# Optimization experiments

Measured on AMD Instinct MI355X. Metric: run time of the kernel, lower is better.

Reference implementation:

```python
import jax, jax.numpy as jnp
import numpy as np

SINKHORN_ITERS = 4
EPS = 1e-6


def setup_inputs() -> dict:
    key = jax.random.key(0)
    B, T, W, D = 2, 4096, 4, 2048
    k1, k2 = jax.random.split(key, 2)
    x = jax.random.normal(k1, (B, T, W, D), dtype=jnp.float32)
    W_router = jax.random.normal(k2, (W * W + 2 * W, D), dtype=jnp.float32) * 0.02
    b_router = jnp.zeros((W * W + 2 * W,), dtype=jnp.float32)
    return {"x": x, "W_router": W_router, "b_router": b_router}


def _sinkhorn(logits):
    # Bistochastic projection: 4 iterations of alternating row/col normalization.
    def body(w, _):
        w = w / jnp.maximum(w.sum(axis=-1, keepdims=True), EPS)
        w = w / jnp.maximum(w.sum(axis=-2, keepdims=True), EPS)
        return w, None
    w, _ = jax.lax.scan(body, jnp.exp(logits), None, length=SINKHORN_ITERS)
    return w


def reference(x, W_router, b_router):
    B, T, W, D = x.shape
    # router input: mean over the width (stream) dim -> (B, T, D)
    routing_input = x.mean(axis=2)
    raw = routing_input @ W_router.T + b_router          # (B, T, W*W + 2W)
    pre = jax.nn.softmax(raw[..., :W], axis=-1)          # (B, T, W)
    post = jax.nn.softmax(raw[..., W:2 * W], axis=-1)    # (B, T, W)
    res_logits = raw[..., 2 * W:].reshape(B, T, W, W)
    # residual_bias buffer: -2 off-diagonal, +2 on diagonal
    idx = jnp.arange(W)
    bias = jnp.full((W, W), -2.0, dtype=x.dtype).at[idx, idx].set(2.0)
    residual = _sinkhorn(res_logits + bias)              # (B, T, W, W)
    # aggregate streams with pre weights, apply op (identity here)
    aggregated = (x * pre[..., None]).sum(axis=2)        # (B, T, D)
    op_out = aggregated                                  # op = identity
    mixed_residual = jnp.einsum('btij,btjd->btid', residual, x)
    return mixed_residual + post[..., None] * op_out[:, :, None, :]
```

## Files before the change

kernel.cpp:

```cpp
#include <hip/hip_runtime.h>


#define SINKHORN_ITERS 4
#define EPSV 1e-6f

__global__ __launch_bounds__(256, 4) void mchc_fused(
    const float* __restrict__ x,
    const float* __restrict__ Wr,
    const float* __restrict__ br,
    float* __restrict__ out)
{
    const int token = blockIdx.x;
    const int tid   = threadIdx.x;
    const int lane  = tid & 63;
    const int wave  = tid >> 6;

    const float4* __restrict__ x4 = (const float4*)(x + (size_t)token * 8192);
    const float4* __restrict__ w4 = (const float4*)Wr;
    float4*       __restrict__ o4 = (float4*)(out + (size_t)token * 8192);

    float4 xa[4], xb[4];
#pragma unroll
    for (int w = 0; w < 4; ++w) {
        xa[w] = x4[w * 512 + tid];
        xb[w] = x4[w * 512 + 256 + tid];
    }

    float4 sa, sb;
    sa.x = xa[0].x + xa[1].x + xa[2].x + xa[3].x;
    sa.y = xa[0].y + xa[1].y + xa[2].y + xa[3].y;
    sa.z = xa[0].z + xa[1].z + xa[2].z + xa[3].z;
    sa.w = xa[0].w + xa[1].w + xa[2].w + xa[3].w;
    sb.x = xb[0].x + xb[1].x + xb[2].x + xb[3].x;
    sb.y = xb[0].y + xb[1].y + xb[2].y + xb[3].y;
    sb.z = xb[0].z + xb[1].z + xb[2].z + xb[3].z;
    sb.w = xb[0].w + xb[1].w + xb[2].w + xb[3].w;

    float p[24];
#pragma unroll
    for (int k = 0; k < 24; ++k) {
        float4 wa = w4[k * 512 + tid];
        float4 wb = w4[k * 512 + 256 + tid];
        p[k] = sa.x * wa.x + sa.y * wa.y + sa.z * wa.z + sa.w * wa.w
             + sb.x * wb.x + sb.y * wb.y + sb.z * wb.z + sb.w * wb.w;
    }

    __shared__ float red[4][24];
    __shared__ float rawbuf[24];
    __shared__ float Mbuf[16];

#pragma unroll
    for (int k = 0; k < 24; ++k) {
        float v = p[k];
        v += __shfl_xor(v, 1);
        v += __shfl_xor(v, 2);
        v += __shfl_xor(v, 4);
        v += __shfl_xor(v, 8);
        v += __shfl_xor(v, 16);
        v += __shfl_xor(v, 32);
        p[k] = v;
    }
    if (lane == 0) {
#pragma unroll
        for (int k = 0; k < 24; ++k) red[wave][k] = p[k];
    }
    __syncthreads();

    if (tid < 24) {
        float r = red[0][tid] + red[1][tid] + red[2][tid] + red[3][tid];
        rawbuf[tid] = 0.25f * r + br[tid];
    }
    __syncthreads();

    if (tid < 16) {
        const int i = tid >> 2, j = tid & 3;

        float r0 = rawbuf[0], r1 = rawbuf[1], r2 = rawbuf[2], r3 = rawbuf[3];
        float mp = fmaxf(fmaxf(r0, r1), fmaxf(r2, r3));
        float sp = __expf(r0 - mp) + __expf(r1 - mp) + __expf(r2 - mp) + __expf(r3 - mp);
        float pre_j = __expf(rawbuf[j] - mp) / sp;

        float q0 = rawbuf[4], q1 = rawbuf[5], q2 = rawbuf[6], q3 = rawbuf[7];
        float mq = fmaxf(fmaxf(q0, q1), fmaxf(q2, q3));
        float sq = __expf(q0 - mq) + __expf(q1 - mq) + __expf(q2 - mq) + __expf(q3 - mq);
        float post_i = __expf(rawbuf[4 + i] - mq) / sq;

        float w = __expf(rawbuf[8 + tid] + ((i == j) ? 2.0f : -2.0f));
#pragma unroll
        for (int it = 0; it < SINKHORN_ITERS; ++it) {
            float rs = w + __shfl_xor(w, 1);
            rs += __shfl_xor(rs, 2);
            w /= fmaxf(rs, EPSV);
            float cs = w + __shfl_xor(w, 4);
            cs += __shfl_xor(cs, 8);
            w /= fmaxf(cs, EPSV);
        }
        Mbuf[tid] = w + post_i * pre_j;
    }
    __syncthreads();

    float M[16];
#pragma unroll
    for (int m = 0; m < 16; ++m) M[m] = Mbuf[m];

#pragma unroll
    for (int i = 0; i < 4; ++i) {
        float m0 = M[i * 4 + 0], m1 = M[i * 4 + 1], m2 = M[i * 4 + 2], m3 = M[i * 4 + 3];
        float4 oa, ob;
        oa.x = m0 * xa[0].x + m1 * xa[1].x + m2 * xa[2].x + m3 * xa[3].x;
        oa.y = m0 * xa[0].y + m1 * xa[1].y + m2 * xa[2].y + m3 * xa[3].y;
        oa.z = m0 * xa[0].z + m1 * xa[1].z + m2 * xa[2].z + m3 * xa[3].z;
        oa.w = m0 * xa[0].w + m1 * xa[1].w + m2 * xa[2].w + m3 * xa[3].w;
        ob.x = m0 * xb[0].x + m1 * xb[1].x + m2 * xb[2].x + m3 * xb[3].x;
        ob.y = m0 * xb[0].y + m1 * xb[1].y + m2 * xb[2].y + m3 * xb[3].y;
        ob.z = m0 * xb[0].z + m1 * xb[1].z + m2 * xb[2].z + m3 * xb[3].z;
        ob.w = m0 * xb[0].w + m1 * xb[1].w + m2 * xb[2].w + m3 * xb[3].w;
        o4[i * 512 + tid]       = oa;
        o4[i * 512 + 256 + tid] = ob;
    }
}

extern "C" void kernel_launch(void* const* d_in, const int* in_sizes, int n_in,
                              void* d_out, int out_size, void* d_ws, size_t ws_size,
                              hipStream_t stream) {
    const float* x  = (const float*)d_in[0];
    const float* Wr = (const float*)d_in[1];
    const float* br = (const float*)d_in[2];
    float* out = (float*)d_out;

    const int tokens = in_sizes[0] / (4 * 2048);
    mchc_fused<<<dim3(tokens), dim3(256), 0, stream>>>(x, Wr, br, out);
}
```

Measured before the change: 516.4 us.

## Process four tokens per block with register prefetch of next token

Each block now handles four consecutive tokens and prefetches the next token's x into registers while computing the current one. The three block barriers per token become one, using a double-buffered shared reduction array, and every wave computes softmax and Sinkhorn redundantly and broadcasts M by shuffle instead of through shared memory. The aim is to hide global load latency and cut synchronisation and launch overhead. The cost is more registers (two x sets), which may reduce occupancy, and four times fewer blocks; the launch assumes the token count is divisible by four.

```diff
diff --git a/kernel.cpp b/kernel.cpp
--- a/kernel.cpp
+++ b/kernel.cpp
@@ -1,7 +1,7 @@
 #include <hip/hip_runtime.h>
 
 
-#define SINKHORN_ITERS 4
+#define NTOK 4
 #define EPSV 1e-6f
 
 __global__ __launch_bounds__(256, 4) void mchc_fused(
@@ -10,113 +10,126 @@
     const float* __restrict__ br,
     float* __restrict__ out)
 {
-    const int token = blockIdx.x;
-    const int tid   = threadIdx.x;
-    const int lane  = tid & 63;
-    const int wave  = tid >> 6;
+    const int tid  = threadIdx.x;
+    const int lane = tid & 63;
+    const int wave = tid >> 6;
+    const int t0   = blockIdx.x * NTOK;
 
-    const float4* __restrict__ x4 = (const float4*)(x + (size_t)token * 8192);
+    __shared__ float red[2][4][24];
+
     const float4* __restrict__ w4 = (const float4*)Wr;
-    float4*       __restrict__ o4 = (float4*)(out + (size_t)token * 8192);
+
+    float brp[8];
+#pragma unroll
+    for (int k = 0; k < 8; ++k) brp[k] = br[k];
+    const int l16 = lane & 15;
+    const int si = l16 >> 2, sj = l16 & 3;
+    const float brw = br[8 + l16];
 
     float4 xa[4], xb[4];
+    float4 ya[4], yb[4];
+    {
+        const float4* xp = (const float4*)(x + (size_t)t0 * 8192);
 #pragma unroll
-    for (int w = 0; w < 4; ++w) {
-        xa[w] = x4[w * 512 + tid];
-        xb[w] = x4[w * 512 + 256 + tid];
+        for (int w = 0; w < 4; ++w) {
+            xa[w] = xp[w * 512 + tid];
+            xb[w] = xp[w * 512 + 256 + tid];
+        }
     }
 
-    float4 sa, sb;
-    sa.x = xa[0].x + xa[1].x + xa[2].x + xa[3].x;
-    sa.y = xa[0].y + xa[1].y + xa[2].y + xa[3].y;
-    sa.z = xa[0].z + xa[1].z + xa[2].z + xa[3].z;
-    sa.w = xa[0].w + xa[1].w + xa[2].w + xa[3].w;
-    sb.x = xb[0].x + xb[1].x + xb[2].x + xb[3].x;
-    sb.y = xb[0].y + xb[1].y + xb[2].y + xb[3].y;
-    sb.z = xb[0].z + xb[1].z + xb[2].z + xb[3].z;
-    sb.w = xb[0].w + xb[1].w + xb[2].w + xb[3].w;
+#pragma unroll
+    for (int n = 0; n < NTOK; ++n) {
+        const int t = t0 + n;
 
-    float p[24];
+        {
+            const int tn = (n + 1 < NTOK) ? (t + 1) : t;
+            const float4* xp = (const float4*)(x + (size_t)tn * 8192);
 #pragma unroll
-    for (int k = 0; k < 24; ++k) {
-        float4 wa = w4[k * 512 + tid];
-        float4 wb = w4[k * 512 + 256 + tid];
-        p[k] = sa.x * wa.x + sa.y * wa.y + sa.z * wa.z + sa.w * wa.w
-             + sb.x * wb.x + sb.y * wb.y + sb.z * wb.z + sb.w * wb.w;
-    }
+            for (int w = 0; w < 4; ++w) {
+                ya[w] = xp[w * 512 + tid];
+                yb[w] = xp[w * 512 + 256 + tid];
+            }
+        }
 
-    __shared__ float red[4][24];
-    __shared__ float rawbuf[24];
-    __shared__ float Mbuf[16];
+        float4 sa, sb;
+        sa.x = xa[0].x + xa[1].x + xa[2].x + xa[3].x;
+        sa.y = xa[0].y + xa[1].y + xa[2].y + xa[3].y;
+        sa.z = xa[0].z + xa[1].z + xa[2].z + xa[3].z;
+        sa.w = xa[0].w + xa[1].w + xa[2].w + xa[3].w;
+        sb.x = xb[0].x + xb[1].x + xb[2].x + xb[3].x;
+        sb.y = xb[0].y + xb[1].y + xb[2].y + xb[3].y;
+        sb.z = xb[0].z + xb[1].z + xb[2].z + xb[3].z;
+        sb.w = xb[0].w + xb[1].w + xb[2].w + xb[3].w;
 
 #pragma unroll
-    for (int k = 0; k < 24; ++k) {
-        float v = p[k];
-        v += __shfl_xor(v, 1);
-        v += __shfl_xor(v, 2);
-        v += __shfl_xor(v, 4);
-        v += __shfl_xor(v, 8);
-        v += __shfl_xor(v, 16);
-        v += __shfl_xor(v, 32);
-        p[k] = v;
-    }
-    if (lane == 0) {
+        for (int k = 0; k < 24; ++k) {
+            float4 wa = w4[k * 512 + tid];
+            float4 wb = w4[k * 512 + 256 + tid];
+            float v = sa.x * wa.x + sa.y * wa.y + sa.z * wa.z + sa.w * wa.w
+                    + sb.x * wb.x + sb.y * wb.y + sb.z * wb.z + sb.w * wb.w;
+            v += __shfl_xor(v, 1);
+            v += __shfl_xor(v, 2);
+            v += __shfl_xor(v, 4);
+            v += __shfl_xor(v, 8);
+            v += __shfl_xor(v, 16);
+            v += __shfl_xor(v, 32);
+            if (lane == 0) red[n & 1][wave][k] = v;
+        }
+
+        asm volatile("s_waitcnt lgkmcnt(0)\n\ts_barrier" ::: "memory");
+
+        const float* rp = &red[n & 1][0][0];
+        float r[8];
 #pragma unroll
-        for (int k = 0; k < 24; ++k) red[wave][k] = p[k];
-    }
-    __syncthreads();
+        for (int k = 0; k < 8; ++k)
+            r[k] = 0.25f * (rp[k] + rp[24 + k] + rp[48 + k] + rp[72 + k]) + brp[k];
+        float rw = 0.25f * (rp[8 + l16] + rp[32 + l16] + rp[56 + l16] + rp[80 + l16]) + brw;
 
-    if (tid < 24) {
-        float r = red[0][tid] + red[1][tid] + red[2][tid] + red[3][tid];
-        rawbuf[tid] = 0.25f * r + br[tid];
-    }
-    __syncthreads();
+        float mp = fmaxf(fmaxf(r[0], r[1]), fmaxf(r[2], r[3]));
+        float e0 = __expf(r[0] - mp), e1 = __expf(r[1] - mp);
+        float e2 = __expf(r[2] - mp), e3 = __expf(r[3] - mp);
+        float sp = e0 + e1 + e2 + e3;
+        float pre_j = ((sj == 0) ? e0 : (sj == 1) ? e1 : (sj == 2) ? e2 : e3) / sp;
 
-    if (tid < 16) {
-        const int i = tid >> 2, j = tid & 3;
+        float mq = fmaxf(fmaxf(r[4], r[5]), fmaxf(r[6], r[7]));
+        float f0 = __expf(r[4] - mq), f1 = __expf(r[5] - mq);
+        float f2 = __expf(r[6] - mq), f3 = __expf(r[7] - mq);
+        float sq = f0 + f1 + f2 + f3;
+        float post_i = ((si == 0) ? f0 : (si == 1) ? f1 : (si == 2) ? f2 : f3) / sq;
 
-        float r0 = rawbuf[0], r1 = rawbuf[1], r2 = rawbuf[2], r3 = rawbuf[3];
-        float mp = fmaxf(fmaxf(r0, r1), fmaxf(r2, r3));
-        float sp = __expf(r0 - mp) + __expf(r1 - mp) + __expf(r2 - mp) + __expf(r3 - mp);
-        float pre_j = __expf(rawbuf[j] - mp) / sp;
+        float wv = __expf(rw + ((si == sj) ? 2.0f : -2.0f));
+#pragma unroll
+        for (int it = 0; it < 4; ++it) {
+            float rs = wv + __shfl_xor(wv, 1); rs += __shfl_xor(rs, 2);
+            wv /= fmaxf(rs, EPSV);
+            float cs = wv + __shfl_xor(wv, 4); cs += __shfl_xor(cs, 8);
+            wv /= fmaxf(cs, EPSV);
+        }
+        float Mv = wv + post_i * pre_j;
 
-        float q0 = rawbuf[4], q1 = rawbuf[5], q2 = rawbuf[6], q3 = rawbuf[7];
-        float mq = fmaxf(fmaxf(q0, q1), fmaxf(q2, q3));
-        float sq = __expf(q0 - mq) + __expf(q1 - mq) + __expf(q2 - mq) + __expf(q3 - mq);
-        float post_i = __expf(rawbuf[4 + i] - mq) / sq;
+        float M[16];
+#pragma unroll
+        for (int m = 0; m < 16; ++m) M[m] = __shfl(Mv, m);
 
-        float w = __expf(rawbuf[8 + tid] + ((i == j) ? 2.0f : -2.0f));
+        float4* __restrict__ o4 = (float4*)(out + (size_t)t * 8192);
 #pragma unroll
-        for (int it = 0; it < SINKHORN_ITERS; ++it) {
-            float rs = w + __shfl_xor(w, 1);
-            rs += __shfl_xor(rs, 2);
-            w /= fmaxf(rs, EPSV);
-            float cs = w + __shfl_xor(w, 4);
-            cs += __shfl_xor(cs, 8);
-            w /= fmaxf(cs, EPSV);
+        for (int i = 0; i < 4; ++i) {
+            float m0 = M[i * 4 + 0], m1 = M[i * 4 + 1], m2 = M[i * 4 + 2], m3 = M[i * 4 + 3];
+            float4 oa, ob;
+            oa.x = m0 * xa[0].x + m1 * xa[1].x + m2 * xa[2].x + m3 * xa[3].x;
+            oa.y = m0 * xa[0].y + m1 * xa[1].y + m2 * xa[2].y + m3 * xa[3].y;
+            oa.z = m0 * xa[0].z + m1 * xa[1].z + m2 * xa[2].z + m3 * xa[3].z;
+            oa.w = m0 * xa[0].w + m1 * xa[1].w + m2 * xa[2].w + m3 * xa[3].w;
+            ob.x = m0 * xb[0].x + m1 * xb[1].x + m2 * xb[2].x + m3 * xb[3].x;
+            ob.y = m0 * xb[0].y + m1 * xb[1].y + m2 * xb[2].y + m3 * xb[3].y;
+            ob.z = m0 * xb[0].z + m1 * xb[1].z + m2 * xb[2].z + m3 * xb[3].z;
+            ob.w = m0 * xb[0].w + m1 * xb[1].w + m2 * xb[2].w + m3 * xb[3].w;
+            o4[i * 512 + tid]       = oa;
+            o4[i * 512 + 256 + tid] = ob;
         }
-        Mbuf[tid] = w + post_i * pre_j;
-    }
-    __syncthreads();
-
-    float M[16];
-#pragma unroll
-    for (int m = 0; m < 16; ++m) M[m] = Mbuf[m];
 
 #pragma unroll
-    for (int i = 0; i < 4; ++i) {
-        float m0 = M[i * 4 + 0], m1 = M[i * 4 + 1], m2 = M[i * 4 + 2], m3 = M[i * 4 + 3];
-        float4 oa, ob;
-        oa.x = m0 * xa[0].x + m1 * xa[1].x + m2 * xa[2].x + m3 * xa[3].x;
-        oa.y = m0 * xa[0].y + m1 * xa[1].y + m2 * xa[2].y + m3 * xa[3].y;
-        oa.z = m0 * xa[0].z + m1 * xa[1].z + m2 * xa[2].z + m3 * xa[3].z;
-        oa.w = m0 * xa[0].w + m1 * xa[1].w + m2 * xa[2].w + m3 * xa[3].w;
-        ob.x = m0 * xb[0].x + m1 * xb[1].x + m2 * xb[2].x + m3 * xb[3].x;
-        ob.y = m0 * xb[0].y + m1 * xb[1].y + m2 * xb[2].y + m3 * xb[3].y;
-        ob.z = m0 * xb[0].z + m1 * xb[1].z + m2 * xb[2].z + m3 * xb[3].z;
-        ob.w = m0 * xb[0].w + m1 * xb[1].w + m2 * xb[2].w + m3 * xb[3].w;
-        o4[i * 512 + tid]       = oa;
-        o4[i * 512 + 256 + tid] = ob;
+        for (int w = 0; w < 4; ++w) { xa[w] = ya[w]; xb[w] = yb[w]; }
     }
 }
 
@@ -129,5 +142,5 @@
     float* out = (float*)d_out;
 
     const int tokens = in_sizes[0] / (4 * 2048);
-    mchc_fused<<<dim3(tokens), dim3(256), 0, stream>>>(x, Wr, br, out);
+    mchc_fused<<<dim3(tokens / NTOK), dim3(256), 0, stream>>>(x, Wr, br, out);
 }
```

Result: slower. 617.3 us (+19.5%).
